# Optimization experiments

Measured on AMD Instinct MI355X. Metric: run time of the kernel, lower is better.

Reference implementation:

```python
import jax, jax.numpy as jnp
import numpy as np

EPS = 1e-5

def layer_norm(x, w, b):
    mu = jnp.mean(x, axis=-1, keepdims=True)
    var = jnp.mean(jnp.square(x - mu), axis=-1, keepdims=True)
    return (x - mu) * jax.lax.rsqrt(var + EPS) * w + b

def setup_inputs() -> dict:
    key = jax.random.key(0)
    ks = jax.random.split(key, 12)
    B, T, C = 4, 2048, 1024
    s = lambda d: 1.0 / np.sqrt(d)
    return {
        "x":      jax.random.normal(ks[0], (B, T, C), dtype=jnp.float32),
        "w_attn": jax.random.normal(ks[1], (C, 3 * C), dtype=jnp.float32) * s(C),
        "b_attn": jnp.zeros((3 * C,), jnp.float32),
        "w_o":    jax.random.normal(ks[2], (C, C), dtype=jnp.float32) * s(C),
        "b_o":    jnp.zeros((C,), jnp.float32),
        "ln_w":   jnp.ones((C,), jnp.float32),
        "ln_b":   jnp.zeros((C,), jnp.float32),
        "w_fc1":  jax.random.normal(ks[3], (C, 4 * C), dtype=jnp.float32) * s(C),
        "b_fc1":  jnp.zeros((4 * C,), jnp.float32),
        "w_fc2":  jax.random.normal(ks[4], (4 * C, C), dtype=jnp.float32) * s(4 * C),
        "b_fc2":  jnp.zeros((C,), jnp.float32),
        "n_heads": 16,
    }

def reference(x, w_attn, b_attn, w_o, b_o, ln_w, ln_b, w_fc1, b_fc1, w_fc2, b_fc2, n_heads):
    B, T, C = x.shape
    H = n_heads
    Dh = C // H
    qkv = x @ w_attn + b_attn                      # [B,T,3C]
    q, k, v = jnp.split(qkv, 3, axis=-1)
    q = q.reshape(B, T, H, Dh).transpose(0, 2, 1, 3)  # [B,H,T,Dh]
    k = k.reshape(B, T, H, Dh).transpose(0, 2, 1, 3)
    v = v.reshape(B, T, H, Dh).transpose(0, 2, 1, 3)
    scores = jnp.einsum("bhtd,bhsd->bhts", q, k) / jnp.sqrt(jnp.float32(Dh))
    w = jax.nn.softmax(scores, axis=-1)            # no causal mask in source
    out = jnp.einsum("bhts,bhsd->bhtd", w, v)      # [B,H,T,Dh]
    out = out.transpose(0, 2, 1, 3).reshape(B, T, C)
    attn_out = out @ w_o + b_o
    x = x + attn_out
    h = layer_norm(x, ln_w, ln_b)
    h = jax.nn.gelu(h @ w_fc1 + b_fc1, approximate=False)
    h = h @ w_fc2 + b_fc2
    return x + h
```

## Files before the change

### kernel.cpp

```cpp
#include <hip/hip_runtime.h>
#include <hip/hip_bf16.h>
#include <math.h>
#include <stdint.h>

typedef __attribute__((ext_vector_type(8))) short s16x8;
typedef __attribute__((ext_vector_type(4))) float f32x4;
typedef __attribute__((ext_vector_type(4))) u_int32_t u32x4;
typedef unsigned int u32;
typedef unsigned short u16;

#define DEVINL __device__ __forceinline__
#define VMW(n) asm volatile("s_waitcnt vmcnt(" #n ")" ::: "memory")

DEVINL u16 f2bf(float f) {
    u32 b = __builtin_bit_cast(u32, f);
    u32 r = (b + 0x7fffu + ((b >> 16) & 1u)) >> 16;
    return (u16)r;
}

DEVINL float fexp2(float x) {
    float r;
    asm("v_exp_f32 %0, %1" : "=v"(r) : "v"(x));
    return r;
}

DEVINL u32 cvt_pk_bf16(float lo, float hi) {
    u32 r;
    asm("v_cvt_pk_bf16_f32 %0, %1, %2" : "=v"(r) : "v"(lo), "v"(hi));
    return r;
}

DEVINL void gload_lds16(const void* g, const void* l) {
    __builtin_amdgcn_global_load_lds(
        (const __attribute__((address_space(1))) u32*)(uintptr_t)g,
        (__attribute__((address_space(3))) u32*)(uintptr_t)l, 16, 0, 0);
}

__global__ __launch_bounds__(256)
void cvt_bf16_kernel(const float* __restrict__ in, u16* __restrict__ out, int n4)
{
    int i = blockIdx.x * 256 + threadIdx.x;
    const int stride = gridDim.x * 256;
    for (; i < n4; i += stride) {
        float4 v = ((const float4*)in)[i];
        ushort4 o;
        o.x = f2bf(v.x); o.y = f2bf(v.y); o.z = f2bf(v.z); o.w = f2bf(v.w);
        ((ushort4*)out)[i] = o;
    }
}

__global__ __launch_bounds__(256)
void transpose_cvt(const float* __restrict__ src, u16* __restrict__ dst, int R, int C)
{
    __shared__ float tile[64][65];
    const int t = threadIdx.x;
    const int c0 = blockIdx.x * 64, r0 = blockIdx.y * 64;
    const int rr = t >> 6;
    const int cc = t & 63;
    #pragma unroll
    for (int i = 0; i < 16; ++i)
        tile[i * 4 + rr][cc] = src[(size_t)(r0 + i * 4 + rr) * C + c0 + cc];
    __syncthreads();
    #pragma unroll
    for (int i = 0; i < 16; ++i) {
        int orow = i * 4 + rr;
        dst[(size_t)(c0 + orow) * R + r0 + cc] = f2bf(tile[cc][orow]);
    }
}

__global__ __launch_bounds__(256)
void vtrans_kernel(const u16* __restrict__ qkv, u16* __restrict__ vt)
{
    __shared__ u16 tile[64][68];
    const int t = threadIdx.x;
    const int st = blockIdx.x;
    const int bh = blockIdx.y;
    const int b = bh >> 4, h = bh & 15;
    const int s0 = st * 64;
    const int rr = t >> 6, cc = t & 63;
    const int sc = (cc & 32) | (((cc >> 2) & 3) << 3) | (((cc >> 4) & 1) << 2) | (cc & 3);
    #pragma unroll
    for (int i = 0; i < 16; ++i) {
        int s = i * 4 + rr;
        tile[s][cc] = qkv[(size_t)(b * 2048 + s0 + s) * 3072 + 2048 + h * 64 + cc];
    }
    __syncthreads();
    #pragma unroll
    for (int i = 0; i < 16; ++i) {
        int d = i * 4 + rr;
        vt[(size_t)(bh * 64 + d) * 2048 + s0 + sc] = tile[cc][d];
    }
}

template<int MODE, int QSC>
__global__ __launch_bounds__(512, 1)
void gemm3s(const u16* __restrict__ A, const u16* __restrict__ B,
            const float* __restrict__ bias, const float* __restrict__ resid,
            u16* __restrict__ obf, float* __restrict__ of32,
            int M, int N, int K)
{
    constexpr int ABYTES = 128 * 128;
    constexpr int BUF = ABYTES + 32768;
    extern __shared__ char lds[];

    const int t = threadIdx.x, lane = t & 63, w = t >> 6;
    const int wr = w >> 2, wc = w & 3, g = lane >> 4, lr = lane & 15;
    const int bm = blockIdx.x * 128, bn = blockIdx.y * 256;

    const int srow = t >> 3;
    const int scol = (((t & 7) ^ (srow & 7)) * 8);
    const u16* ag = A + (size_t)(bm + srow) * K + scol;
    const u16* bg = B + (size_t)(bn + srow) * K + scol;

    f32x4 acc[4][4] = {};

    auto STAGE = [&](int tt) {
        char* bb = lds + (tt % 3) * BUF;
        const size_t ko = (size_t)tt * 64;
        #pragma unroll
        for (int L = 0; L < 2; ++L)
            gload_lds16(ag + (size_t)L * 64 * K + ko, bb + L * 8192 + t * 16);
        #pragma unroll
        for (int L = 0; L < 4; ++L)
            gload_lds16(bg + (size_t)L * 64 * K + ko, bb + ABYTES + L * 8192 + t * 16);
    };

    const int NT = K >> 6;
    STAGE(0); STAGE(1);

    const int xr = (lr & 7) << 4;

    for (int tt = 0; tt < NT; ++tt) {
        if (tt < NT - 1) { VMW(6); } else { VMW(0); }
        __builtin_amdgcn_s_barrier();
        asm volatile("" ::: "memory");
        if (tt + 2 < NT) STAGE(tt + 2);

        const char* cbuf = lds + (tt % 3) * BUF;
        s16x8 af[4][2], bf4[4][2];
        #pragma unroll
        for (int mf = 0; mf < 4; ++mf) {
            const int arow = wr * 64 + mf * 16 + lr;
            #pragma unroll
            for (int ks = 0; ks < 2; ++ks)
                af[mf][ks] = *(const s16x8*)(cbuf + arow * 128 + ((ks * 64 + g * 16) ^ xr));
        }
        #pragma unroll
        for (int nf = 0; nf < 4; ++nf) {
            const int brow = wc * 64 + nf * 16 + lr;
            #pragma unroll
            for (int ks = 0; ks < 2; ++ks)
                bf4[nf][ks] = *(const s16x8*)(cbuf + ABYTES + brow * 128 + ((ks * 64 + g * 16) ^ xr));
        }
        __builtin_amdgcn_s_setprio(1);
        #pragma unroll
        for (int ks = 0; ks < 2; ++ks)
            #pragma unroll
            for (int mf = 0; mf < 4; ++mf)
                #pragma unroll
                for (int nf = 0; nf < 4; ++nf)
                    acc[mf][nf] = __builtin_amdgcn_mfma_f32_16x16x32_bf16(
                        af[mf][ks], bf4[nf][ks], acc[mf][nf], 0, 0, 0);
        __builtin_amdgcn_s_setprio(0);
    }

    #pragma unroll
    for (int mf = 0; mf < 4; ++mf) {
        const int rbase = bm + wr * 64 + mf * 16 + g * 4;
        #pragma unroll
        for (int nf = 0; nf < 4; ++nf) {
            const int col = bn + wc * 64 + nf * 16 + lr;
            const float bia = bias[col];
            #pragma unroll
            for (int b2 = 0; b2 < 4; ++b2) {
                const int r = rbase + b2;
                float v = acc[mf][nf][b2] + bia;
                if (QSC && col < 1024) v *= 0.18033688011112042f;
                if (MODE == 1) v = 0.5f * v * (1.0f + erff(v * 0.70710678118654752f));
                if (MODE == 2) {
                    v += resid[(size_t)r * N + col];
                    of32[(size_t)r * N + col] = v;
                } else {
                    obf[(size_t)r * N + col] = f2bf(v);
                }
            }
        }
    }
}

__global__ __launch_bounds__(256)
void attn_kernel(const u16* __restrict__ qkv, const u16* __restrict__ vt,
                 u16* __restrict__ attnb)
{
    __shared__ u16 Kls[2][4096];
    __shared__ u16 Vls[2][4096];
    const int t = threadIdx.x, lane = t & 63, w = t >> 6;
    const int g = lane >> 4, lr = lane & 15;
    const int wg = blockIdx.x;
    const int xcd = wg & 7, slot = wg >> 3;
    const int bh = xcd * 8 + (slot >> 5);
    const int qt = slot & 31;
    const int b = bh >> 4, h = bh & 15;

    const int srow = t >> 3;
    const int scol = (((t & 7) ^ (srow & 7)) * 8);
    const u16* kg0 = qkv + (size_t)(b * 2048 + srow) * 3072 + 1024 + h * 64 + scol;
    const u16* kg1 = qkv + (size_t)(b * 2048 + srow + 32) * 3072 + 1024 + h * 64 + scol;
    const u16* vg0 = vt + (size_t)(bh * 64 + srow) * 2048 + scol;
    const u16* vg1 = vt + (size_t)(bh * 64 + srow + 32) * 2048 + scol;
    const int ldst = w * 512;

    gload_lds16(kg0, &Kls[0][ldst]);
    gload_lds16(kg1, &Kls[0][2048 + ldst]);
    gload_lds16(vg0, &Vls[0][ldst]);
    gload_lds16(vg1, &Vls[0][2048 + ldst]);

    const int qtok = b * 2048 + qt * 64 + w * 16 + lr;
    const u16* qp = qkv + (size_t)qtok * 3072 + h * 64;
    const s16x8 qf0 = *(const s16x8*)(qp + g * 8);
    const s16x8 qf1 = *(const s16x8*)(qp + 32 + g * 8);

    f32x4 o[4] = {};
    float psum = 0.f;
    const int xr = (lr & 7) * 8;

    for (int s = 0; s < 32; ++s) {
        const int cur = s & 1;
        __syncthreads();
        if (s + 1 < 32) {
            const size_t ko = (size_t)(s + 1) * 64;
            gload_lds16(kg0 + ko * 3072, &Kls[cur ^ 1][ldst]);
            gload_lds16(kg1 + ko * 3072, &Kls[cur ^ 1][2048 + ldst]);
            gload_lds16(vg0 + ko, &Vls[cur ^ 1][ldst]);
            gload_lds16(vg1 + ko, &Vls[cur ^ 1][2048 + ldst]);
        }

        f32x4 sv[4];
        #pragma unroll
        for (int n = 0; n < 4; ++n) {
            const int kr = (n * 16 + lr) * 64;
            const s16x8 k0v = *(const s16x8*)&Kls[cur][kr + ((g * 8) ^ xr)];
            const s16x8 k1v = *(const s16x8*)&Kls[cur][kr + ((32 + g * 8) ^ xr)];
            f32x4 z = {};
            z = __builtin_amdgcn_mfma_f32_16x16x32_bf16(k0v, qf0, z, 0, 0, 0);
            z = __builtin_amdgcn_mfma_f32_16x16x32_bf16(k1v, qf1, z, 0, 0, 0);
            sv[n] = z;
        }

        float p[4][4];
        #pragma unroll
        for (int n = 0; n < 4; ++n) {
            #pragma unroll
            for (int b2 = 0; b2 < 4; ++b2)
                p[n][b2] = fexp2(sv[n][b2]);
            psum += (p[n][0] + p[n][1]) + (p[n][2] + p[n][3]);
        }

        u32x4 pk0, pk1;
        pk0[0] = cvt_pk_bf16(p[0][0], p[0][1]);
        pk0[1] = cvt_pk_bf16(p[0][2], p[0][3]);
        pk0[2] = cvt_pk_bf16(p[1][0], p[1][1]);
        pk0[3] = cvt_pk_bf16(p[1][2], p[1][3]);
        pk1[0] = cvt_pk_bf16(p[2][0], p[2][1]);
        pk1[1] = cvt_pk_bf16(p[2][2], p[2][3]);
        pk1[2] = cvt_pk_bf16(p[3][0], p[3][1]);
        pk1[3] = cvt_pk_bf16(p[3][2], p[3][3]);
        const s16x8 pa0 = __builtin_bit_cast(s16x8, pk0);
        const s16x8 pa1 = __builtin_bit_cast(s16x8, pk1);

        #pragma unroll
        for (int n = 0; n < 4; ++n) {
            const int vr = (n * 16 + lr) * 64;
            const s16x8 v0 = *(const s16x8*)&Vls[cur][vr + ((g * 8) ^ xr)];
            const s16x8 v1 = *(const s16x8*)&Vls[cur][vr + ((32 + g * 8) ^ xr)];
            o[n] = __builtin_amdgcn_mfma_f32_16x16x32_bf16(pa0, v0, o[n], 0, 0, 0);
            o[n] = __builtin_amdgcn_mfma_f32_16x16x32_bf16(pa1, v1, o[n], 0, 0, 0);
        }
    }

    psum += __shfl_xor(psum, 16);
    psum += __shfl_xor(psum, 32);
    const int orow0 = b * 2048 + qt * 64 + w * 16 + g * 4;
    #pragma unroll
    for (int b2 = 0; b2 < 4; ++b2) {
        const float inv = 1.0f / __shfl(psum, g * 4 + b2);
        #pragma unroll
        for (int n = 0; n < 4; ++n)
            attnb[(size_t)(orow0 + b2) * 1024 + h * 64 + n * 16 + lr] = f2bf(o[n][b2] * inv);
    }
}

__global__ __launch_bounds__(256)
void ln_kernel(const float* __restrict__ x, const float* __restrict__ lw,
               const float* __restrict__ lb, u16* __restrict__ out)
{
    const int row = blockIdx.x;
    const int t = threadIdx.x;
    const float4 v = ((const float4*)(x + (size_t)row * 1024))[t];
    float s = v.x + v.y + v.z + v.w;
    float s2 = v.x * v.x + v.y * v.y + v.z * v.z + v.w * v.w;
    #pragma unroll
    for (int m = 32; m >= 1; m >>= 1) {
        s  += __shfl_xor(s, m);
        s2 += __shfl_xor(s2, m);
    }
    __shared__ float red[16];
    const int w = t >> 6, lane = t & 63;
    if (lane == 0) { red[w] = s; red[8 + w] = s2; }
    __syncthreads();
    s  = red[0] + red[1] + red[2] + red[3];
    s2 = red[8] + red[9] + red[10] + red[11];
    const float mu = s * (1.0f / 1024.0f);
    const float var = s2 * (1.0f / 1024.0f) - mu * mu;
    const float inv = rsqrtf(var + 1e-5f);
    const float4 wv = ((const float4*)lw)[t];
    const float4 bv = ((const float4*)lb)[t];
    ushort4 oo;
    oo.x = f2bf((v.x - mu) * inv * wv.x + bv.x);
    oo.y = f2bf((v.y - mu) * inv * wv.y + bv.y);
    oo.z = f2bf((v.z - mu) * inv * wv.z + bv.z);
    oo.w = f2bf((v.w - mu) * inv * wv.w + bv.w);
    ((ushort4*)(out + (size_t)row * 1024))[t] = oo;
}

extern "C" void kernel_launch(void* const* d_in, const int* in_sizes, int n_in,
                              void* d_out, int out_size, void* d_ws, size_t ws_size,
                              hipStream_t stream)
{
    const float* x      = (const float*)d_in[0];
    const float* w_attn = (const float*)d_in[1];
    const float* b_attn = (const float*)d_in[2];
    const float* w_o    = (const float*)d_in[3];
    const float* b_o    = (const float*)d_in[4];
    const float* ln_w   = (const float*)d_in[5];
    const float* ln_b   = (const float*)d_in[6];
    const float* w_fc1  = (const float*)d_in[7];
    const float* b_fc1  = (const float*)d_in[8];
    const float* w_fc2  = (const float*)d_in[9];
    const float* b_fc2  = (const float*)d_in[10];
    float* out = (float*)d_out;

    char* ws = (char*)d_ws;
    u16*   xb    = (u16*)(ws);
    u16*   wqkvT = (u16*)(ws + 16777216);
    u16*   woT   = (u16*)(ws + 23068672);
    u16*   w1T   = (u16*)(ws + 25165824);
    u16*   w2T   = (u16*)(ws + 33554432);
    float* x1    = (float*)(ws + 41943040);
    u16*   attnb = (u16*)(ws + 75497472);
    u16*   hb    = attnb;
    u16*   qkvb  = (u16*)(ws + 92274688);
    u16*   vtb   = qkvb + 25165824;
    u16*   h1    = qkvb;

    cvt_bf16_kernel<<<2048, 256, 0, stream>>>(x, xb, 8192 * 1024 / 4);
    transpose_cvt<<<dim3(48, 16), 256, 0, stream>>>(w_attn, wqkvT, 1024, 3072);
    transpose_cvt<<<dim3(16, 16), 256, 0, stream>>>(w_o,   woT,  1024, 1024);
    transpose_cvt<<<dim3(64, 16), 256, 0, stream>>>(w_fc1, w1T,  1024, 4096);
    transpose_cvt<<<dim3(16, 64), 256, 0, stream>>>(w_fc2, w2T,  4096, 1024);

    gemm3s<0, 1><<<dim3(64, 12), 512, 147456, stream>>>(xb, wqkvT, b_attn, nullptr,
                                                        qkvb, nullptr, 8192, 3072, 1024);
    vtrans_kernel<<<dim3(32, 64), 256, 0, stream>>>(qkvb, vtb);
    attn_kernel<<<2048, 256, 0, stream>>>(qkvb, vtb, attnb);
    gemm3s<2, 0><<<dim3(64, 4), 512, 147456, stream>>>(attnb, woT, b_o, x,
                                                       nullptr, x1, 8192, 1024, 1024);
    ln_kernel<<<8192, 256, 0, stream>>>(x1, ln_w, ln_b, hb);
    gemm3s<1, 0><<<dim3(64, 16), 512, 147456, stream>>>(hb, w1T, b_fc1, nullptr,
                                                        h1, nullptr, 8192, 4096, 1024);
    gemm3s<2, 0><<<dim3(64, 4), 512, 147456, stream>>>(h1, w2T, b_fc2, x1,
                                                       nullptr, out, 8192, 1024, 4096);
}
```

Before: 417.0 us.

## Replace triple-buffered GEMM with double-buffered variant and 256-row tile for FC1

```diff
diff --git a/kernel.cpp b/kernel.cpp
--- a/kernel.cpp
+++ b/kernel.cpp
@@ -11,6 +11,7 @@
 
 #define DEVINL __device__ __forceinline__
 #define VMW(n) asm volatile("s_waitcnt vmcnt(" #n ")" ::: "memory")
+#define CFENCE asm volatile("" ::: "memory")
 
 DEVINL u16 f2bf(float f) {
     u32 b = __builtin_bit_cast(u32, f);
@@ -92,55 +93,47 @@
     }
 }
 
-template<int MODE, int QSC>
+template<int BM, int MODE, int QSC>
 __global__ __launch_bounds__(512, 1)
-void gemm3s(const u16* __restrict__ A, const u16* __restrict__ B,
+void gemmdb(const u16* __restrict__ A, const u16* __restrict__ B,
             const float* __restrict__ bias, const float* __restrict__ resid,
             u16* __restrict__ obf, float* __restrict__ of32,
             int M, int N, int K)
 {
-    constexpr int ABYTES = 128 * 128;
+    constexpr int MF = BM / 32;
+    constexpr int AL = BM / 64;
+    constexpr int ABYTES = BM * 128;
     constexpr int BUF = ABYTES + 32768;
     extern __shared__ char lds[];
 
     const int t = threadIdx.x, lane = t & 63, w = t >> 6;
     const int wr = w >> 2, wc = w & 3, g = lane >> 4, lr = lane & 15;
-    const int bm = blockIdx.x * 128, bn = blockIdx.y * 256;
+    const int bm = blockIdx.x * BM, bn = blockIdx.y * 256;
 
     const int srow = t >> 3;
     const int scol = (((t & 7) ^ (srow & 7)) * 8);
     const u16* ag = A + (size_t)(bm + srow) * K + scol;
     const u16* bg = B + (size_t)(bn + srow) * K + scol;
 
-    f32x4 acc[4][4] = {};
-
-    auto STAGE = [&](int tt) {
-        char* bb = lds + (tt % 3) * BUF;
+    f32x4 acc[MF][4] = {};
+
+    auto STAGE = [&](int tt, char* bb) {
         const size_t ko = (size_t)tt * 64;
         #pragma unroll
-        for (int L = 0; L < 2; ++L)
+        for (int L = 0; L < AL; ++L)
             gload_lds16(ag + (size_t)L * 64 * K + ko, bb + L * 8192 + t * 16);
         #pragma unroll
         for (int L = 0; L < 4; ++L)
             gload_lds16(bg + (size_t)L * 64 * K + ko, bb + ABYTES + L * 8192 + t * 16);
     };
 
-    const int NT = K >> 6;
-    STAGE(0); STAGE(1);
-
     const int xr = (lr & 7) << 4;
 
-    for (int tt = 0; tt < NT; ++tt) {
-        if (tt < NT - 1) { VMW(6); } else { VMW(0); }
-        __builtin_amdgcn_s_barrier();
-        asm volatile("" ::: "memory");
-        if (tt + 2 < NT) STAGE(tt + 2);
-
-        const char* cbuf = lds + (tt % 3) * BUF;
-        s16x8 af[4][2], bf4[4][2];
-        #pragma unroll
-        for (int mf = 0; mf < 4; ++mf) {
-            const int arow = wr * 64 + mf * 16 + lr;
+    auto COMPUTE = [&](const char* cbuf) {
+        s16x8 af[MF][2], bf4[4][2];
+        #pragma unroll
+        for (int mf = 0; mf < MF; ++mf) {
+            const int arow = wr * (BM / 2) + mf * 16 + lr;
             #pragma unroll
             for (int ks = 0; ks < 2; ++ks)
                 af[mf][ks] = *(const s16x8*)(cbuf + arow * 128 + ((ks * 64 + g * 16) ^ xr));
@@ -156,17 +149,42 @@
         #pragma unroll
         for (int ks = 0; ks < 2; ++ks)
             #pragma unroll
-            for (int mf = 0; mf < 4; ++mf)
+            for (int mf = 0; mf < MF; ++mf)
                 #pragma unroll
                 for (int nf = 0; nf < 4; ++nf)
                     acc[mf][nf] = __builtin_amdgcn_mfma_f32_16x16x32_bf16(
                         af[mf][ks], bf4[nf][ks], acc[mf][nf], 0, 0, 0);
         __builtin_amdgcn_s_setprio(0);
-    }
-
-    #pragma unroll
-    for (int mf = 0; mf < 4; ++mf) {
-        const int rbase = bm + wr * 64 + mf * 16 + g * 4;
+    };
+
+    const int NT = K >> 6;
+    STAGE(0, lds);
+
+    for (int tt = 0; tt < NT; tt += 2) {
+        __builtin_amdgcn_s_barrier();
+        CFENCE;
+        if (tt + 1 < NT) {
+            STAGE(tt + 1, lds + BUF);
+            if constexpr (BM == 256) { VMW(8); } else { VMW(6); }
+        } else { VMW(0); }
+        __builtin_amdgcn_s_barrier();
+        __builtin_amdgcn_sched_barrier(0);
+        COMPUTE(lds);
+
+        __builtin_amdgcn_s_barrier();
+        CFENCE;
+        if (tt + 2 < NT) {
+            STAGE(tt + 2, lds);
+            if constexpr (BM == 256) { VMW(8); } else { VMW(6); }
+        } else { VMW(0); }
+        __builtin_amdgcn_s_barrier();
+        __builtin_amdgcn_sched_barrier(0);
+        COMPUTE(lds + BUF);
+    }
+
+    #pragma unroll
+    for (int mf = 0; mf < MF; ++mf) {
+        const int rbase = bm + wr * (BM / 2) + mf * 16 + g * 4;
         #pragma unroll
         for (int nf = 0; nf < 4; ++nf) {
             const int col = bn + wc * 64 + nf * 16 + lr;
@@ -359,15 +377,15 @@
     transpose_cvt<<<dim3(64, 16), 256, 0, stream>>>(w_fc1, w1T,  1024, 4096);
     transpose_cvt<<<dim3(16, 64), 256, 0, stream>>>(w_fc2, w2T,  4096, 1024);
 
-    gemm3s<0, 1><<<dim3(64, 12), 512, 147456, stream>>>(xb, wqkvT, b_attn, nullptr,
-                                                        qkvb, nullptr, 8192, 3072, 1024);
+    gemmdb<128, 0, 1><<<dim3(64, 12), 512, 98304, stream>>>(xb, wqkvT, b_attn, nullptr,
+                                                            qkvb, nullptr, 8192, 3072, 1024);
     vtrans_kernel<<<dim3(32, 64), 256, 0, stream>>>(qkvb, vtb);
     attn_kernel<<<2048, 256, 0, stream>>>(qkvb, vtb, attnb);
-    gemm3s<2, 0><<<dim3(64, 4), 512, 147456, stream>>>(attnb, woT, b_o, x,
-                                                       nullptr, x1, 8192, 1024, 1024);
+    gemmdb<128, 2, 0><<<dim3(64, 4), 512, 98304, stream>>>(attnb, woT, b_o, x,
+                                                           nullptr, x1, 8192, 1024, 1024);
     ln_kernel<<<8192, 256, 0, stream>>>(x1, ln_w, ln_b, hb);
-    gemm3s<1, 0><<<dim3(64, 16), 512, 147456, stream>>>(hb, w1T, b_fc1, nullptr,
-                                                        h1, nullptr, 8192, 4096, 1024);
-    gemm3s<2, 0><<<dim3(64, 4), 512, 147456, stream>>>(h1, w2T, b_fc2, x1,
-                                                       nullptr, out, 8192, 1024, 4096);
-}
+    gemmdb<256, 1, 0><<<dim3(32, 16), 512, 131072, stream>>>(hb, w1T, b_fc1, nullptr,
+                                                             h1, nullptr, 8192, 4096, 1024);
+    gemmdb<128, 2, 0><<<dim3(64, 4), 512, 98304, stream>>>(h1, w2T, b_fc2, x1,
+                                                           nullptr, out, 8192, 1024, 4096);
+}
```

After: 515.2 us. +23.5%, slower.

## Swizzle GEMM block order across XCDs and double attention query tile per block

Applied to the files above, without the earlier changes.

```diff
diff --git a/kernel.cpp b/kernel.cpp
--- a/kernel.cpp
+++ b/kernel.cpp
@@ -105,7 +105,9 @@
 
     const int t = threadIdx.x, lane = t & 63, w = t >> 6;
     const int wr = w >> 2, wc = w & 3, g = lane >> 4, lr = lane & 15;
-    const int bm = blockIdx.x * 128, bn = blockIdx.y * 256;
+    const int id = blockIdx.x;
+    const int bm = (((id & 7) << 3) | ((id >> 3) & 7)) * 128;
+    const int bn = (id >> 6) * 256;
 
     const int srow = t >> 3;
     const int scol = (((t & 7) ^ (srow & 7)) * 8);
@@ -188,7 +190,7 @@
     }
 }
 
-__global__ __launch_bounds__(256)
+__global__ __launch_bounds__(512)
 void attn_kernel(const u16* __restrict__ qkv, const u16* __restrict__ vt,
                  u16* __restrict__ attnb)
 {
@@ -198,24 +200,19 @@
     const int g = lane >> 4, lr = lane & 15;
     const int wg = blockIdx.x;
     const int xcd = wg & 7, slot = wg >> 3;
-    const int bh = xcd * 8 + (slot >> 5);
-    const int qt = slot & 31;
+    const int bh = xcd * 8 + (slot >> 4);
+    const int qt = slot & 15;
     const int b = bh >> 4, h = bh & 15;
 
     const int srow = t >> 3;
     const int scol = (((t & 7) ^ (srow & 7)) * 8);
-    const u16* kg0 = qkv + (size_t)(b * 2048 + srow) * 3072 + 1024 + h * 64 + scol;
-    const u16* kg1 = qkv + (size_t)(b * 2048 + srow + 32) * 3072 + 1024 + h * 64 + scol;
-    const u16* vg0 = vt + (size_t)(bh * 64 + srow) * 2048 + scol;
-    const u16* vg1 = vt + (size_t)(bh * 64 + srow + 32) * 2048 + scol;
-    const int ldst = w * 512;
-
-    gload_lds16(kg0, &Kls[0][ldst]);
-    gload_lds16(kg1, &Kls[0][2048 + ldst]);
-    gload_lds16(vg0, &Vls[0][ldst]);
-    gload_lds16(vg1, &Vls[0][2048 + ldst]);
-
-    const int qtok = b * 2048 + qt * 64 + w * 16 + lr;
+    const u16* kg = qkv + (size_t)(b * 2048 + srow) * 3072 + 1024 + h * 64 + scol;
+    const u16* vg = vt + (size_t)(bh * 64 + srow) * 2048 + scol;
+
+    gload_lds16(kg, &Kls[0][t * 8]);
+    gload_lds16(vg, &Vls[0][t * 8]);
+
+    const int qtok = b * 2048 + qt * 128 + w * 16 + lr;
     const u16* qp = qkv + (size_t)qtok * 3072 + h * 64;
     const s16x8 qf0 = *(const s16x8*)(qp + g * 8);
     const s16x8 qf1 = *(const s16x8*)(qp + 32 + g * 8);
@@ -229,10 +226,8 @@
         __syncthreads();
         if (s + 1 < 32) {
             const size_t ko = (size_t)(s + 1) * 64;
-            gload_lds16(kg0 + ko * 3072, &Kls[cur ^ 1][ldst]);
-            gload_lds16(kg1 + ko * 3072, &Kls[cur ^ 1][2048 + ldst]);
-            gload_lds16(vg0 + ko, &Vls[cur ^ 1][ldst]);
-            gload_lds16(vg1 + ko, &Vls[cur ^ 1][2048 + ldst]);
+            gload_lds16(kg + ko * 3072, &Kls[cur ^ 1][t * 8]);
+            gload_lds16(vg + ko, &Vls[cur ^ 1][t * 8]);
         }
 
         f32x4 sv[4];
@@ -280,7 +275,7 @@
 
     psum += __shfl_xor(psum, 16);
     psum += __shfl_xor(psum, 32);
-    const int orow0 = b * 2048 + qt * 64 + w * 16 + g * 4;
+    const int orow0 = b * 2048 + qt * 128 + w * 16 + g * 4;
     #pragma unroll
     for (int b2 = 0; b2 < 4; ++b2) {
         const float inv = 1.0f / __shfl(psum, g * 4 + b2);
@@ -359,15 +354,15 @@
     transpose_cvt<<<dim3(64, 16), 256, 0, stream>>>(w_fc1, w1T,  1024, 4096);
     transpose_cvt<<<dim3(16, 64), 256, 0, stream>>>(w_fc2, w2T,  4096, 1024);
 
-    gemm3s<0, 1><<<dim3(64, 12), 512, 147456, stream>>>(xb, wqkvT, b_attn, nullptr,
-                                                        qkvb, nullptr, 8192, 3072, 1024);
+    gemm3s<0, 1><<<768, 512, 147456, stream>>>(xb, wqkvT, b_attn, nullptr,
+                                               qkvb, nullptr, 8192, 3072, 1024);
     vtrans_kernel<<<dim3(32, 64), 256, 0, stream>>>(qkvb, vtb);
-    attn_kernel<<<2048, 256, 0, stream>>>(qkvb, vtb, attnb);
-    gemm3s<2, 0><<<dim3(64, 4), 512, 147456, stream>>>(attnb, woT, b_o, x,
-                                                       nullptr, x1, 8192, 1024, 1024);
+    attn_kernel<<<1024, 512, 0, stream>>>(qkvb, vtb, attnb);
+    gemm3s<2, 0><<<256, 512, 147456, stream>>>(attnb, woT, b_o, x,
+                                               nullptr, x1, 8192, 1024, 1024);
     ln_kernel<<<8192, 256, 0, stream>>>(x1, ln_w, ln_b, hb);
-    gemm3s<1, 0><<<dim3(64, 16), 512, 147456, stream>>>(hb, w1T, b_fc1, nullptr,
-                                                        h1, nullptr, 8192, 4096, 1024);
-    gemm3s<2, 0><<<dim3(64, 4), 512, 147456, stream>>>(h1, w2T, b_fc2, x1,
-                                                       nullptr, out, 8192, 1024, 4096);
-}
+    gemm3s<1, 0><<<1024, 512, 147456, stream>>>(hb, w1T, b_fc1, nullptr,
+                                                h1, nullptr, 8192, 4096, 1024);
+    gemm3s<2, 0><<<256, 512, 147456, stream>>>(h1, w2T, b_fc2, x1,
+                                               nullptr, out, 8192, 1024, 4096);
+}
```

Measured after the change: 412.6 us. Within noise of the previous version (-1.1%).
